# Optimization experiments

Hardware: AMD Instinct MI355X
Metric: run time of the kernel (lower is better)

Reference implementation:

```python
import jax, jax.numpy as jnp
import numpy as np
import math


def setup_inputs() -> dict:
    key = jax.random.key(0)
    kq, kk, kv = jax.random.split(key, 3)
    shape = (4, 16, 2048, 64)  # [B, H, S, D]
    return {
        "q": jax.random.normal(kq, shape, dtype=jnp.float32),
        "k": jax.random.normal(kk, shape, dtype=jnp.float32),
        "v": jax.random.normal(kv, shape, dtype=jnp.float32),
    }


def reference(q, k, v):
    # Faithful to the torch module: exp(QK^T / sqrt(d)) then row-normalize
    # (no max-subtraction, matching the original math exactly).
    d = q.shape[-1]
    a = jnp.einsum('bhid,bhjd->bhij', q, k)          # [B,H,S,S]
    a = jnp.exp(a / jnp.float32(math.sqrt(float(d))))
    d_inv = 1.0 / jnp.sum(a, axis=-1, keepdims=True)  # [B,H,S,1]
    a_hat = d_inv * a
    return jnp.einsum('bhij,bhjd->bhid', a_hat, v)   # [B,H,S,D]
```

## Files before the change

kernel.cpp:

```cpp
#include <hip/hip_runtime.h>
#include <hip/hip_fp16.h>

typedef _Float16 half8  __attribute__((ext_vector_type(8)));
typedef _Float16 half4  __attribute__((ext_vector_type(4)));
typedef __fp16   fp16x2 __attribute__((ext_vector_type(2)));
typedef float    floatx4 __attribute__((ext_vector_type(4)));
typedef float    f32x16 __attribute__((ext_vector_type(16)));
typedef unsigned int uint2v __attribute__((ext_vector_type(2)));
typedef unsigned int uint4v __attribute__((ext_vector_type(4)));

#define SEQ    2048
#define HD     64
#define QTILE  256
#define KVB    64
#define PITCH  72
#define NXCD   8

__global__ __launch_bounds__(256, 2)
void attn_fwd(const float* __restrict__ Q, const float* __restrict__ K,
              const float* __restrict__ V, float* __restrict__ O) {
    const int nqt  = SEQ / QTILE;

    const int bid  = blockIdx.x;
    const int xcd  = bid & (NXCD - 1);
    const int slot = bid >> 3;
    const int work = xcd * ((int)gridDim.x >> 3) + slot;
    const int head = work / nqt;
    const int qti  = work % nqt;

    const size_t hoff = (size_t)head * SEQ * HD;
    const float* Qh = Q + hoff;
    const float* Kh = K + hoff;
    const float* Vh = V + hoff;
    float*       Oh = O + hoff;

    const int tid  = threadIdx.x;
    const int lane = tid & 63;
    const int w    = tid >> 6;
    const int l31  = lane & 31;
    const int h    = lane >> 5;
    const int lg   = lane >> 4;
    const int lm   = lane & 15;

    __shared__ __align__(16) _Float16 lds[2][2][KVB][PITCH];

    const int q0w = qti * QTILE + w * 64;

    const int kr  = tid >> 4;
    const int kc  = (tid & 15) << 2;
    const int vr0 = w * 16 + lg * 4;

    const float QSCALE = 0.125f * 1.44269504f;
    half8 qf[2][4];
    #pragma unroll
    for (int set = 0; set < 2; ++set) {
        const float* qp = Qh + (size_t)(q0w + set*32 + l31) * HD + h*8;
        #pragma unroll
        for (int ks = 0; ks < 4; ++ks) {
            floatx4 a = *(const floatx4*)(qp + ks*16);
            floatx4 b = *(const floatx4*)(qp + ks*16 + 4);
            fp16x2 h0 = __builtin_amdgcn_cvt_pkrtz(a[0]*QSCALE, a[1]*QSCALE);
            fp16x2 h1 = __builtin_amdgcn_cvt_pkrtz(a[2]*QSCALE, a[3]*QSCALE);
            fp16x2 h2 = __builtin_amdgcn_cvt_pkrtz(b[0]*QSCALE, b[1]*QSCALE);
            fp16x2 h3 = __builtin_amdgcn_cvt_pkrtz(b[2]*QSCALE, b[3]*QSCALE);
            half8 hh;
            hh[0]=h0[0]; hh[1]=h0[1]; hh[2]=h1[0]; hh[3]=h1[1];
            hh[4]=h2[0]; hh[5]=h2[1]; hh[6]=h3[0]; hh[7]=h3[1];
            qf[set][ks] = hh;
        }
    }

    f32x16 Oa00 = {}, Oa01 = {}, Oa10 = {}, Oa11 = {};
    float ps0 = 0.f, ps1 = 0.f;

    floatx4 kp0, kp1, kp2, kp3;
    floatx4 vp0, vp1, vp2, vp3;

#define ISSUE(KV)                                                            \
    do {                                                                     \
        const float* kbp = Kh + (size_t)(KV) * HD;                           \
        kp0 = *(const floatx4*)(kbp + ( 0 + kr)*HD + kc);                    \
        kp1 = *(const floatx4*)(kbp + (16 + kr)*HD + kc);                    \
        kp2 = *(const floatx4*)(kbp + (32 + kr)*HD + kc);                    \
        kp3 = *(const floatx4*)(kbp + (48 + kr)*HD + kc);                    \
        const float* vbp = Vh + (size_t)(KV) * HD;                           \
        vp0[0] = vbp[(vr0+0)*HD +  0 + lm]; vp0[1] = vbp[(vr0+1)*HD +  0 + lm]; \
        vp0[2] = vbp[(vr0+2)*HD +  0 + lm]; vp0[3] = vbp[(vr0+3)*HD +  0 + lm]; \
        vp1[0] = vbp[(vr0+0)*HD + 16 + lm]; vp1[1] = vbp[(vr0+1)*HD + 16 + lm]; \
        vp1[2] = vbp[(vr0+2)*HD + 16 + lm]; vp1[3] = vbp[(vr0+3)*HD + 16 + lm]; \
        vp2[0] = vbp[(vr0+0)*HD + 32 + lm]; vp2[1] = vbp[(vr0+1)*HD + 32 + lm]; \
        vp2[2] = vbp[(vr0+2)*HD + 32 + lm]; vp2[3] = vbp[(vr0+3)*HD + 32 + lm]; \
        vp3[0] = vbp[(vr0+0)*HD + 48 + lm]; vp3[1] = vbp[(vr0+1)*HD + 48 + lm]; \
        vp3[2] = vbp[(vr0+2)*HD + 48 + lm]; vp3[3] = vbp[(vr0+3)*HD + 48 + lm]; \
    } while (0)

#define STORE_K(KB, REG, QUARTER)                                            \
    do {                                                                     \
        fp16x2 h0 = __builtin_amdgcn_cvt_pkrtz((REG)[0], (REG)[1]);          \
        fp16x2 h1 = __builtin_amdgcn_cvt_pkrtz((REG)[2], (REG)[3]);          \
        half4 kh; kh[0]=h0[0]; kh[1]=h0[1]; kh[2]=h1[0]; kh[3]=h1[1];        \
        *(half4*)&(KB)[((QUARTER)*16 + kr)*PITCH + kc] = kh;                 \
    } while (0)

#define STORE_V(VB, REG, QUARTER)                                            \
    do {                                                                     \
        fp16x2 h0 = __builtin_amdgcn_cvt_pkrtz((REG)[0], (REG)[1]);          \
        fp16x2 h1 = __builtin_amdgcn_cvt_pkrtz((REG)[2], (REG)[3]);          \
        half4 vh; vh[0]=h0[0]; vh[1]=h0[1]; vh[2]=h1[0]; vh[3]=h1[1];        \
        *(half4*)&(VB)[((QUARTER)*16 + lm)*PITCH + vr0] = vh;                \
    } while (0)

#define STORE_ALL(BUF)                                                       \
    do {                                                                     \
        _Float16* Kb_ = &lds[BUF][0][0][0];                                  \
        _Float16* Vb_ = &lds[BUF][1][0][0];                                  \
        STORE_K(Kb_, kp0, 0); STORE_K(Kb_, kp1, 1);                          \
        STORE_K(Kb_, kp2, 2); STORE_K(Kb_, kp3, 3);                          \
        STORE_V(Vb_, vp0, 0); STORE_V(Vb_, vp1, 1);                          \
        STORE_V(Vb_, vp2, 2); STORE_V(Vb_, vp3, 3);                          \
    } while (0)

#define EXP2(X) __builtin_amdgcn_exp2f(X)

#define EXPPACK(S, PW, PSUM)                                                 \
    do {                                                                     \
        float e0_=EXP2((S)[ 0]), e1_=EXP2((S)[ 1]), e2_=EXP2((S)[ 2]), e3_=EXP2((S)[ 3]); \
        float e4_=EXP2((S)[ 4]), e5_=EXP2((S)[ 5]), e6_=EXP2((S)[ 6]), e7_=EXP2((S)[ 7]); \
        float e8_=EXP2((S)[ 8]), e9_=EXP2((S)[ 9]), ea_=EXP2((S)[10]), eb_=EXP2((S)[11]); \
        float ec_=EXP2((S)[12]), ed_=EXP2((S)[13]), ee_=EXP2((S)[14]), ef_=EXP2((S)[15]); \
        PSUM += ((e0_+e1_)+(e2_+e3_)) + ((e4_+e5_)+(e6_+e7_))                \
              + ((e8_+e9_)+(ea_+eb_)) + ((ec_+ed_)+(ee_+ef_));               \
        unsigned x0_ = __builtin_bit_cast(unsigned, __builtin_amdgcn_cvt_pkrtz(e0_, e1_)); \
        unsigned x1_ = __builtin_bit_cast(unsigned, __builtin_amdgcn_cvt_pkrtz(e2_, e3_)); \
        unsigned y0_ = __builtin_bit_cast(unsigned, __builtin_amdgcn_cvt_pkrtz(e4_, e5_)); \
        unsigned y1_ = __builtin_bit_cast(unsigned, __builtin_amdgcn_cvt_pkrtz(e6_, e7_)); \
        unsigned z0_ = __builtin_bit_cast(unsigned, __builtin_amdgcn_cvt_pkrtz(e8_, e9_)); \
        unsigned z1_ = __builtin_bit_cast(unsigned, __builtin_amdgcn_cvt_pkrtz(ea_, eb_)); \
        unsigned u0_ = __builtin_bit_cast(unsigned, __builtin_amdgcn_cvt_pkrtz(ec_, ed_)); \
        unsigned u1_ = __builtin_bit_cast(unsigned, __builtin_amdgcn_cvt_pkrtz(ee_, ef_)); \
        uint2v r0_ = __builtin_amdgcn_permlane32_swap(x0_, y0_, false, false); \
        uint2v r1_ = __builtin_amdgcn_permlane32_swap(x1_, y1_, false, false); \
        uint2v r2_ = __builtin_amdgcn_permlane32_swap(z0_, u0_, false, false); \
        uint2v r3_ = __builtin_amdgcn_permlane32_swap(z1_, u1_, false, false); \
        PW[0] = r0_[0]; PW[1] = r1_[0]; PW[2] = r0_[1]; PW[3] = r1_[1];      \
        PW[4] = r2_[0]; PW[5] = r3_[0]; PW[6] = r2_[1]; PW[7] = r3_[1];      \
    } while (0)

    ISSUE(0);
    STORE_ALL(0);

    for (int kv = 0; kv < SEQ; kv += KVB) {
        const int buf = (kv >> 6) & 1;

        __syncthreads();

        {
            const int kvn = (kv + KVB < SEQ) ? (kv + KVB) : kv;
            ISSUE(kvn);
        }

        const _Float16* Kb = &lds[buf][0][0][0];
        const _Float16* Vb = &lds[buf][1][0][0];

        #pragma unroll
        for (int kb = 0; kb < 2; ++kb) {
            f32x16 s0 = {}, s1 = {};
            __builtin_amdgcn_s_setprio(1);
            #pragma unroll
            for (int ks = 0; ks < 4; ++ks) {
                half8 kf = *(const half8*)&Kb[(kb*32 + l31)*PITCH + ks*16 + h*8];
                s0 = __builtin_amdgcn_mfma_f32_32x32x16_f16(kf, qf[0][ks], s0, 0, 0, 0);
                s1 = __builtin_amdgcn_mfma_f32_32x32x16_f16(kf, qf[1][ks], s1, 0, 0, 0);
            }
            __builtin_amdgcn_s_setprio(0);

            unsigned pw0[8], pw1[8];
            EXPPACK(s0, pw0, ps0);
            EXPPACK(s1, pw1, ps1);

            __builtin_amdgcn_s_setprio(1);
            #pragma unroll
            for (int kh2 = 0; kh2 < 2; ++kh2) {
                const int ks = kb*2 + kh2;
                half8 vb0 = *(const half8*)&Vb[( 0 + l31)*PITCH + ks*16 + h*8];
                half8 vb1 = *(const half8*)&Vb[(32 + l31)*PITCH + ks*16 + h*8];
                uint4v a0 = { pw0[kh2*4+0], pw0[kh2*4+1], pw0[kh2*4+2], pw0[kh2*4+3] };
                uint4v a1 = { pw1[kh2*4+0], pw1[kh2*4+1], pw1[kh2*4+2], pw1[kh2*4+3] };
                half8 pa0 = __builtin_bit_cast(half8, a0);
                half8 pa1 = __builtin_bit_cast(half8, a1);
                Oa00 = __builtin_amdgcn_mfma_f32_32x32x16_f16(pa0, vb0, Oa00, 0, 0, 0);
                Oa01 = __builtin_amdgcn_mfma_f32_32x32x16_f16(pa0, vb1, Oa01, 0, 0, 0);
                Oa10 = __builtin_amdgcn_mfma_f32_32x32x16_f16(pa1, vb0, Oa10, 0, 0, 0);
                Oa11 = __builtin_amdgcn_mfma_f32_32x32x16_f16(pa1, vb1, Oa11, 0, 0, 0);
            }
            __builtin_amdgcn_s_setprio(0);
        }

        STORE_ALL(buf ^ 1);
    }
#undef ISSUE
#undef STORE_K
#undef STORE_V
#undef STORE_ALL
#undef EXPPACK
#undef EXP2

    ps0 += __shfl_xor(ps0, 32, 64);
    ps1 += __shfl_xor(ps1, 32, 64);

    #pragma unroll
    for (int r = 0; r < 16; ++r) {
        const int co = (r & 3) + 8*(r >> 2);
        float inv0 = 1.0f / __shfl(ps0, co + 4*h, 64);
        float inv1 = 1.0f / __shfl(ps1, co + 4*h, 64);
        const size_t row0 = (size_t)(q0w +      co + 4*h) * HD;
        const size_t row1 = (size_t)(q0w + 32 + co + 4*h) * HD;
        Oh[row0 +  0 + l31] = Oa00[r] * inv0;
        Oh[row0 + 32 + l31] = Oa01[r] * inv0;
        Oh[row1 +  0 + l31] = Oa10[r] * inv1;
        Oh[row1 + 32 + l31] = Oa11[r] * inv1;
    }
}

extern "C" void kernel_launch(void* const* d_in, const int* in_sizes, int n_in,
                              void* d_out, int out_size, void* d_ws, size_t ws_size,
                              hipStream_t stream) {
    const float* q = (const float*)d_in[0];
    const float* k = (const float*)d_in[1];
    const float* v = (const float*)d_in[2];
    float* o = (float*)d_out;
    int nheads  = in_sizes[0] / (SEQ * HD);
    int nblocks = nheads * (SEQ / QTILE);
    attn_fwd<<<nblocks, 256, 0, stream>>>(q, k, v, o);
}
```

Baseline: 88.47 us.

## Split global prefetch into phases interleaved with MFMA stages using workgroup barriers

Unrolls the per-tile loop into four explicit phases (QK half A, PV half A, QK half B, PV half B) and splits the next tile's global K/V prefetch into three pieces issued between them. Extra s_barrier calls after each phase keep the waves in lockstep, so memory loads from one wave overlap MFMA work from others in a ping-pong style. The main __syncthreads moves to after the LDS store. This adds several barriers per iteration and raises register pressure from preloading LDS fragments, which could stall waves or cut occupancy.

```diff
diff --git a/kernel.cpp b/kernel.cpp
--- a/kernel.cpp
+++ b/kernel.cpp
@@ -76,18 +76,27 @@
     floatx4 kp0, kp1, kp2, kp3;
     floatx4 vp0, vp1, vp2, vp3;
 
-#define ISSUE(KV)                                                            \
+#define ISSUE_K(KV)                                                          \
     do {                                                                     \
         const float* kbp = Kh + (size_t)(KV) * HD;                           \
         kp0 = *(const floatx4*)(kbp + ( 0 + kr)*HD + kc);                    \
         kp1 = *(const floatx4*)(kbp + (16 + kr)*HD + kc);                    \
         kp2 = *(const floatx4*)(kbp + (32 + kr)*HD + kc);                    \
         kp3 = *(const floatx4*)(kbp + (48 + kr)*HD + kc);                    \
+    } while (0)
+
+#define ISSUE_V1(KV)                                                         \
+    do {                                                                     \
         const float* vbp = Vh + (size_t)(KV) * HD;                           \
         vp0[0] = vbp[(vr0+0)*HD +  0 + lm]; vp0[1] = vbp[(vr0+1)*HD +  0 + lm]; \
         vp0[2] = vbp[(vr0+2)*HD +  0 + lm]; vp0[3] = vbp[(vr0+3)*HD +  0 + lm]; \
         vp1[0] = vbp[(vr0+0)*HD + 16 + lm]; vp1[1] = vbp[(vr0+1)*HD + 16 + lm]; \
         vp1[2] = vbp[(vr0+2)*HD + 16 + lm]; vp1[3] = vbp[(vr0+3)*HD + 16 + lm]; \
+    } while (0)
+
+#define ISSUE_V2(KV)                                                         \
+    do {                                                                     \
+        const float* vbp = Vh + (size_t)(KV) * HD;                           \
         vp2[0] = vbp[(vr0+0)*HD + 32 + lm]; vp2[1] = vbp[(vr0+1)*HD + 32 + lm]; \
         vp2[2] = vbp[(vr0+2)*HD + 32 + lm]; vp2[3] = vbp[(vr0+3)*HD + 32 + lm]; \
         vp3[0] = vbp[(vr0+0)*HD + 48 + lm]; vp3[1] = vbp[(vr0+1)*HD + 48 + lm]; \
@@ -146,59 +155,125 @@
         PW[4] = r2_[0]; PW[5] = r3_[0]; PW[6] = r2_[1]; PW[7] = r3_[1];      \
     } while (0)
 
-    ISSUE(0);
+    ISSUE_K(0); ISSUE_V1(0); ISSUE_V2(0);
     STORE_ALL(0);
+    __syncthreads();
 
     for (int kv = 0; kv < SEQ; kv += KVB) {
         const int buf = (kv >> 6) & 1;
-
-        __syncthreads();
-
-        {
-            const int kvn = (kv + KVB < SEQ) ? (kv + KVB) : kv;
-            ISSUE(kvn);
-        }
+        const int kvn = (kv + KVB < SEQ) ? (kv + KVB) : kv;
 
         const _Float16* Kb = &lds[buf][0][0][0];
         const _Float16* Vb = &lds[buf][1][0][0];
 
-        #pragma unroll
-        for (int kb = 0; kb < 2; ++kb) {
+        unsigned pw0[8], pw1[8], pw2[8], pw3[8];
+
+        {
+            half8 kA0 = *(const half8*)&Kb[( 0 + l31)*PITCH + 0*16 + h*8];
+            half8 kA1 = *(const half8*)&Kb[( 0 + l31)*PITCH + 1*16 + h*8];
+            half8 kA2 = *(const half8*)&Kb[( 0 + l31)*PITCH + 2*16 + h*8];
+            half8 kA3 = *(const half8*)&Kb[( 0 + l31)*PITCH + 3*16 + h*8];
+            ISSUE_K(kvn);
+            __builtin_amdgcn_s_barrier();
             f32x16 s0 = {}, s1 = {};
             __builtin_amdgcn_s_setprio(1);
-            #pragma unroll
-            for (int ks = 0; ks < 4; ++ks) {
-                half8 kf = *(const half8*)&Kb[(kb*32 + l31)*PITCH + ks*16 + h*8];
-                s0 = __builtin_amdgcn_mfma_f32_32x32x16_f16(kf, qf[0][ks], s0, 0, 0, 0);
-                s1 = __builtin_amdgcn_mfma_f32_32x32x16_f16(kf, qf[1][ks], s1, 0, 0, 0);
-            }
+            s0 = __builtin_amdgcn_mfma_f32_32x32x16_f16(kA0, qf[0][0], s0, 0, 0, 0);
+            s1 = __builtin_amdgcn_mfma_f32_32x32x16_f16(kA0, qf[1][0], s1, 0, 0, 0);
+            s0 = __builtin_amdgcn_mfma_f32_32x32x16_f16(kA1, qf[0][1], s0, 0, 0, 0);
+            s1 = __builtin_amdgcn_mfma_f32_32x32x16_f16(kA1, qf[1][1], s1, 0, 0, 0);
+            s0 = __builtin_amdgcn_mfma_f32_32x32x16_f16(kA2, qf[0][2], s0, 0, 0, 0);
+            s1 = __builtin_amdgcn_mfma_f32_32x32x16_f16(kA2, qf[1][2], s1, 0, 0, 0);
+            s0 = __builtin_amdgcn_mfma_f32_32x32x16_f16(kA3, qf[0][3], s0, 0, 0, 0);
+            s1 = __builtin_amdgcn_mfma_f32_32x32x16_f16(kA3, qf[1][3], s1, 0, 0, 0);
             __builtin_amdgcn_s_setprio(0);
-
-            unsigned pw0[8], pw1[8];
+            __builtin_amdgcn_s_barrier();
+
             EXPPACK(s0, pw0, ps0);
             EXPPACK(s1, pw1, ps1);
-
+        }
+        {
+            half8 vA0 = *(const half8*)&Vb[( 0 + l31)*PITCH + 0*16 + h*8];
+            half8 vA1 = *(const half8*)&Vb[(32 + l31)*PITCH + 0*16 + h*8];
+            half8 vA2 = *(const half8*)&Vb[( 0 + l31)*PITCH + 1*16 + h*8];
+            half8 vA3 = *(const half8*)&Vb[(32 + l31)*PITCH + 1*16 + h*8];
+            ISSUE_V1(kvn);
+            __builtin_amdgcn_s_barrier();
+            uint4v a0 = { pw0[0], pw0[1], pw0[2], pw0[3] };
+            uint4v a1 = { pw1[0], pw1[1], pw1[2], pw1[3] };
+            uint4v b0 = { pw0[4], pw0[5], pw0[6], pw0[7] };
+            uint4v b1 = { pw1[4], pw1[5], pw1[6], pw1[7] };
+            half8 pa0 = __builtin_bit_cast(half8, a0);
+            half8 pa1 = __builtin_bit_cast(half8, a1);
+            half8 pb0 = __builtin_bit_cast(half8, b0);
+            half8 pb1 = __builtin_bit_cast(half8, b1);
             __builtin_amdgcn_s_setprio(1);
-            #pragma unroll
-            for (int kh2 = 0; kh2 < 2; ++kh2) {
-                const int ks = kb*2 + kh2;
-                half8 vb0 = *(const half8*)&Vb[( 0 + l31)*PITCH + ks*16 + h*8];
-                half8 vb1 = *(const half8*)&Vb[(32 + l31)*PITCH + ks*16 + h*8];
-                uint4v a0 = { pw0[kh2*4+0], pw0[kh2*4+1], pw0[kh2*4+2], pw0[kh2*4+3] };
-                uint4v a1 = { pw1[kh2*4+0], pw1[kh2*4+1], pw1[kh2*4+2], pw1[kh2*4+3] };
-                half8 pa0 = __builtin_bit_cast(half8, a0);
-                half8 pa1 = __builtin_bit_cast(half8, a1);
-                Oa00 = __builtin_amdgcn_mfma_f32_32x32x16_f16(pa0, vb0, Oa00, 0, 0, 0);
-                Oa01 = __builtin_amdgcn_mfma_f32_32x32x16_f16(pa0, vb1, Oa01, 0, 0, 0);
-                Oa10 = __builtin_amdgcn_mfma_f32_32x32x16_f16(pa1, vb0, Oa10, 0, 0, 0);
-                Oa11 = __builtin_amdgcn_mfma_f32_32x32x16_f16(pa1, vb1, Oa11, 0, 0, 0);
-            }
+            Oa00 = __builtin_amdgcn_mfma_f32_32x32x16_f16(pa0, vA0, Oa00, 0, 0, 0);
+            Oa01 = __builtin_amdgcn_mfma_f32_32x32x16_f16(pa0, vA1, Oa01, 0, 0, 0);
+            Oa10 = __builtin_amdgcn_mfma_f32_32x32x16_f16(pa1, vA0, Oa10, 0, 0, 0);
+            Oa11 = __builtin_amdgcn_mfma_f32_32x32x16_f16(pa1, vA1, Oa11, 0, 0, 0);
+            Oa00 = __builtin_amdgcn_mfma_f32_32x32x16_f16(pb0, vA2, Oa00, 0, 0, 0);
+            Oa01 = __builtin_amdgcn_mfma_f32_32x32x16_f16(pb0, vA3, Oa01, 0, 0, 0);
+            Oa10 = __builtin_amdgcn_mfma_f32_32x32x16_f16(pb1, vA2, Oa10, 0, 0, 0);
+            Oa11 = __builtin_amdgcn_mfma_f32_32x32x16_f16(pb1, vA3, Oa11, 0, 0, 0);
             __builtin_amdgcn_s_setprio(0);
+            __builtin_amdgcn_s_barrier();
+        }
+
+        {
+            half8 kB0 = *(const half8*)&Kb[(32 + l31)*PITCH + 0*16 + h*8];
+            half8 kB1 = *(const half8*)&Kb[(32 + l31)*PITCH + 1*16 + h*8];
+            half8 kB2 = *(const half8*)&Kb[(32 + l31)*PITCH + 2*16 + h*8];
+            half8 kB3 = *(const half8*)&Kb[(32 + l31)*PITCH + 3*16 + h*8];
+            ISSUE_V2(kvn);
+            __builtin_amdgcn_s_barrier();
+            f32x16 s2 = {}, s3 = {};
+            __builtin_amdgcn_s_setprio(1);
+            s2 = __builtin_amdgcn_mfma_f32_32x32x16_f16(kB0, qf[0][0], s2, 0, 0, 0);
+            s3 = __builtin_amdgcn_mfma_f32_32x32x16_f16(kB0, qf[1][0], s3, 0, 0, 0);
+            s2 = __builtin_amdgcn_mfma_f32_32x32x16_f16(kB1, qf[0][1], s2, 0, 0, 0);
+            s3 = __builtin_amdgcn_mfma_f32_32x32x16_f16(kB1, qf[1][1], s3, 0, 0, 0);
+            s2 = __builtin_amdgcn_mfma_f32_32x32x16_f16(kB2, qf[0][2], s2, 0, 0, 0);
+            s3 = __builtin_amdgcn_mfma_f32_32x32x16_f16(kB2, qf[1][2], s3, 0, 0, 0);
+            s2 = __builtin_amdgcn_mfma_f32_32x32x16_f16(kB3, qf[0][3], s2, 0, 0, 0);
+            s3 = __builtin_amdgcn_mfma_f32_32x32x16_f16(kB3, qf[1][3], s3, 0, 0, 0);
+            __builtin_amdgcn_s_setprio(0);
+            __builtin_amdgcn_s_barrier();
+
+            EXPPACK(s2, pw2, ps0);
+            EXPPACK(s3, pw3, ps1);
+        }
+        {
+            half8 vB0 = *(const half8*)&Vb[( 0 + l31)*PITCH + 2*16 + h*8];
+            half8 vB1 = *(const half8*)&Vb[(32 + l31)*PITCH + 2*16 + h*8];
+            half8 vB2 = *(const half8*)&Vb[( 0 + l31)*PITCH + 3*16 + h*8];
+            half8 vB3 = *(const half8*)&Vb[(32 + l31)*PITCH + 3*16 + h*8];
+            __builtin_amdgcn_s_barrier();
+            uint4v a0 = { pw2[0], pw2[1], pw2[2], pw2[3] };
+            uint4v a1 = { pw3[0], pw3[1], pw3[2], pw3[3] };
+            uint4v b0 = { pw2[4], pw2[5], pw2[6], pw2[7] };
+            uint4v b1 = { pw3[4], pw3[5], pw3[6], pw3[7] };
+            half8 pa0 = __builtin_bit_cast(half8, a0);
+            half8 pa1 = __builtin_bit_cast(half8, a1);
+            half8 pb0 = __builtin_bit_cast(half8, b0);
+            half8 pb1 = __builtin_bit_cast(half8, b1);
+            __builtin_amdgcn_s_setprio(1);
+            Oa00 = __builtin_amdgcn_mfma_f32_32x32x16_f16(pa0, vB0, Oa00, 0, 0, 0);
+            Oa01 = __builtin_amdgcn_mfma_f32_32x32x16_f16(pa0, vB1, Oa01, 0, 0, 0);
+            Oa10 = __builtin_amdgcn_mfma_f32_32x32x16_f16(pa1, vB0, Oa10, 0, 0, 0);
+            Oa11 = __builtin_amdgcn_mfma_f32_32x32x16_f16(pa1, vB1, Oa11, 0, 0, 0);
+            Oa00 = __builtin_amdgcn_mfma_f32_32x32x16_f16(pb0, vB2, Oa00, 0, 0, 0);
+            Oa01 = __builtin_amdgcn_mfma_f32_32x32x16_f16(pb0, vB3, Oa01, 0, 0, 0);
+            Oa10 = __builtin_amdgcn_mfma_f32_32x32x16_f16(pb1, vB2, Oa10, 0, 0, 0);
+            Oa11 = __builtin_amdgcn_mfma_f32_32x32x16_f16(pb1, vB3, Oa11, 0, 0, 0);
+            __builtin_amdgcn_s_setprio(0);
         }
 
         STORE_ALL(buf ^ 1);
+        __syncthreads();
     }
-#undef ISSUE
+#undef ISSUE_K
+#undef ISSUE_V1
+#undef ISSUE_V2
 #undef STORE_K
 #undef STORE_V
 #undef STORE_ALL
```

After: 91.44 us. 1.03x slower.

## Double KV block to 128 and split global loads into two half-stages

Applied to the files above, without the earlier changes.

Raises the KV tile from 64 to 128 rows, so each iteration needs one barrier instead of two per 128 keys. Global loads for the next tile are issued in two halves, each overlapped with two 32-key compute sub-blocks and then stored to the other LDS buffer. V is stored transposed in a single wider-pitch array. LDS use roughly doubles, to about 72KB per block, which may limit the two-blocks-per-CU occupancy target, and the V pitch of 136 may cause bank conflicts.

```diff
diff --git a/kernel.cpp b/kernel.cpp
--- a/kernel.cpp
+++ b/kernel.cpp
@@ -12,8 +12,9 @@
 #define SEQ    2048
 #define HD     64
 #define QTILE  256
-#define KVB    64
-#define PITCH  72
+#define KVB    128
+#define KP     72
+#define VP     136
 #define NXCD   8
 
 __global__ __launch_bounds__(256, 2)
@@ -42,7 +43,8 @@
     const int lg   = lane >> 4;
     const int lm   = lane & 15;
 
-    __shared__ __align__(16) _Float16 lds[2][2][KVB][PITCH];
+    __shared__ __align__(16) _Float16 Klds[2][KVB][KP];
+    __shared__ __align__(16) _Float16 Vlds[2][HD][VP];
 
     const int q0w = qti * QTILE + w * 64;
 
@@ -76,14 +78,14 @@
     floatx4 kp0, kp1, kp2, kp3;
     floatx4 vp0, vp1, vp2, vp3;
 
-#define ISSUE(KV)                                                            \
-    do {                                                                     \
-        const float* kbp = Kh + (size_t)(KV) * HD;                           \
+#define ISSUE_H(KV, HALF)                                                    \
+    do {                                                                     \
+        const float* kbp = Kh + (size_t)((KV) + (HALF)*64) * HD;             \
         kp0 = *(const floatx4*)(kbp + ( 0 + kr)*HD + kc);                    \
         kp1 = *(const floatx4*)(kbp + (16 + kr)*HD + kc);                    \
         kp2 = *(const floatx4*)(kbp + (32 + kr)*HD + kc);                    \
         kp3 = *(const floatx4*)(kbp + (48 + kr)*HD + kc);                    \
-        const float* vbp = Vh + (size_t)(KV) * HD;                           \
+        const float* vbp = Vh + (size_t)((KV) + (HALF)*64) * HD;             \
         vp0[0] = vbp[(vr0+0)*HD +  0 + lm]; vp0[1] = vbp[(vr0+1)*HD +  0 + lm]; \
         vp0[2] = vbp[(vr0+2)*HD +  0 + lm]; vp0[3] = vbp[(vr0+3)*HD +  0 + lm]; \
         vp1[0] = vbp[(vr0+0)*HD + 16 + lm]; vp1[1] = vbp[(vr0+1)*HD + 16 + lm]; \
@@ -94,30 +96,42 @@
         vp3[2] = vbp[(vr0+2)*HD + 48 + lm]; vp3[3] = vbp[(vr0+3)*HD + 48 + lm]; \
     } while (0)
 
-#define STORE_K(KB, REG, QUARTER)                                            \
-    do {                                                                     \
-        fp16x2 h0 = __builtin_amdgcn_cvt_pkrtz((REG)[0], (REG)[1]);          \
-        fp16x2 h1 = __builtin_amdgcn_cvt_pkrtz((REG)[2], (REG)[3]);          \
-        half4 kh; kh[0]=h0[0]; kh[1]=h0[1]; kh[2]=h1[0]; kh[3]=h1[1];        \
-        *(half4*)&(KB)[((QUARTER)*16 + kr)*PITCH + kc] = kh;                 \
-    } while (0)
-
-#define STORE_V(VB, REG, QUARTER)                                            \
-    do {                                                                     \
-        fp16x2 h0 = __builtin_amdgcn_cvt_pkrtz((REG)[0], (REG)[1]);          \
-        fp16x2 h1 = __builtin_amdgcn_cvt_pkrtz((REG)[2], (REG)[3]);          \
-        half4 vh; vh[0]=h0[0]; vh[1]=h0[1]; vh[2]=h1[0]; vh[3]=h1[1];        \
-        *(half4*)&(VB)[((QUARTER)*16 + lm)*PITCH + vr0] = vh;                \
-    } while (0)
-
-#define STORE_ALL(BUF)                                                       \
-    do {                                                                     \
-        _Float16* Kb_ = &lds[BUF][0][0][0];                                  \
-        _Float16* Vb_ = &lds[BUF][1][0][0];                                  \
-        STORE_K(Kb_, kp0, 0); STORE_K(Kb_, kp1, 1);                          \
-        STORE_K(Kb_, kp2, 2); STORE_K(Kb_, kp3, 3);                          \
-        STORE_V(Vb_, vp0, 0); STORE_V(Vb_, vp1, 1);                          \
-        STORE_V(Vb_, vp2, 2); STORE_V(Vb_, vp3, 3);                          \
+#define STORE_H(BUF, HALF)                                                   \
+    do {                                                                     \
+        _Float16* Kb_ = &Klds[BUF][(HALF)*64][0];                            \
+        _Float16* Vb_ = &Vlds[BUF][0][0];                                    \
+        { fp16x2 h0 = __builtin_amdgcn_cvt_pkrtz(kp0[0], kp0[1]);            \
+          fp16x2 h1 = __builtin_amdgcn_cvt_pkrtz(kp0[2], kp0[3]);            \
+          half4 kh; kh[0]=h0[0]; kh[1]=h0[1]; kh[2]=h1[0]; kh[3]=h1[1];      \
+          *(half4*)&Kb_[( 0 + kr)*KP + kc] = kh; }                           \
+        { fp16x2 h0 = __builtin_amdgcn_cvt_pkrtz(kp1[0], kp1[1]);            \
+          fp16x2 h1 = __builtin_amdgcn_cvt_pkrtz(kp1[2], kp1[3]);            \
+          half4 kh; kh[0]=h0[0]; kh[1]=h0[1]; kh[2]=h1[0]; kh[3]=h1[1];      \
+          *(half4*)&Kb_[(16 + kr)*KP + kc] = kh; }                           \
+        { fp16x2 h0 = __builtin_amdgcn_cvt_pkrtz(kp2[0], kp2[1]);            \
+          fp16x2 h1 = __builtin_amdgcn_cvt_pkrtz(kp2[2], kp2[3]);            \
+          half4 kh; kh[0]=h0[0]; kh[1]=h0[1]; kh[2]=h1[0]; kh[3]=h1[1];      \
+          *(half4*)&Kb_[(32 + kr)*KP + kc] = kh; }                           \
+        { fp16x2 h0 = __builtin_amdgcn_cvt_pkrtz(kp3[0], kp3[1]);            \
+          fp16x2 h1 = __builtin_amdgcn_cvt_pkrtz(kp3[2], kp3[3]);            \
+          half4 kh; kh[0]=h0[0]; kh[1]=h0[1]; kh[2]=h1[0]; kh[3]=h1[1];      \
+          *(half4*)&Kb_[(48 + kr)*KP + kc] = kh; }                           \
+        { fp16x2 h0 = __builtin_amdgcn_cvt_pkrtz(vp0[0], vp0[1]);            \
+          fp16x2 h1 = __builtin_amdgcn_cvt_pkrtz(vp0[2], vp0[3]);            \
+          half4 vh; vh[0]=h0[0]; vh[1]=h0[1]; vh[2]=h1[0]; vh[3]=h1[1];      \
+          *(half4*)&Vb_[( 0 + lm)*VP + (HALF)*64 + vr0] = vh; }              \
+        { fp16x2 h0 = __builtin_amdgcn_cvt_pkrtz(vp1[0], vp1[1]);            \
+          fp16x2 h1 = __builtin_amdgcn_cvt_pkrtz(vp1[2], vp1[3]);            \
+          half4 vh; vh[0]=h0[0]; vh[1]=h0[1]; vh[2]=h1[0]; vh[3]=h1[1];      \
+          *(half4*)&Vb_[(16 + lm)*VP + (HALF)*64 + vr0] = vh; }              \
+        { fp16x2 h0 = __builtin_amdgcn_cvt_pkrtz(vp2[0], vp2[1]);            \
+          fp16x2 h1 = __builtin_amdgcn_cvt_pkrtz(vp2[2], vp2[3]);            \
+          half4 vh; vh[0]=h0[0]; vh[1]=h0[1]; vh[2]=h1[0]; vh[3]=h1[1];      \
+          *(half4*)&Vb_[(32 + lm)*VP + (HALF)*64 + vr0] = vh; }              \
+        { fp16x2 h0 = __builtin_amdgcn_cvt_pkrtz(vp3[0], vp3[1]);            \
+          fp16x2 h1 = __builtin_amdgcn_cvt_pkrtz(vp3[2], vp3[3]);            \
+          half4 vh; vh[0]=h0[0]; vh[1]=h0[1]; vh[2]=h1[0]; vh[3]=h1[1];      \
+          *(half4*)&Vb_[(48 + lm)*VP + (HALF)*64 + vr0] = vh; }              \
     } while (0)
 
 #define EXP2(X) __builtin_amdgcn_exp2f(X)
@@ -146,64 +160,66 @@
         PW[4] = r2_[0]; PW[5] = r3_[0]; PW[6] = r2_[1]; PW[7] = r3_[1];      \
     } while (0)
 
-    ISSUE(0);
-    STORE_ALL(0);
+#define COMPUTE_KB(KB)                                                       \
+    do {                                                                     \
+        f32x16 s0 = {}, s1 = {};                                             \
+        __builtin_amdgcn_s_setprio(1);                                       \
+        _Pragma("unroll")                                                    \
+        for (int ks = 0; ks < 4; ++ks) {                                     \
+            half8 kf = *(const half8*)&Kb[((KB)*32 + l31)*KP + ks*16 + h*8]; \
+            s0 = __builtin_amdgcn_mfma_f32_32x32x16_f16(kf, qf[0][ks], s0, 0, 0, 0); \
+            s1 = __builtin_amdgcn_mfma_f32_32x32x16_f16(kf, qf[1][ks], s1, 0, 0, 0); \
+        }                                                                    \
+        __builtin_amdgcn_s_setprio(0);                                       \
+        unsigned pw0[8], pw1[8];                                             \
+        EXPPACK(s0, pw0, ps0);                                               \
+        EXPPACK(s1, pw1, ps1);                                               \
+        __builtin_amdgcn_s_setprio(1);                                       \
+        _Pragma("unroll")                                                    \
+        for (int kh2 = 0; kh2 < 2; ++kh2) {                                  \
+            const int ks = (KB)*2 + kh2;                                     \
+            half8 vb0 = *(const half8*)&Vb[( 0 + l31)*VP + ks*16 + h*8];     \
+            half8 vb1 = *(const half8*)&Vb[(32 + l31)*VP + ks*16 + h*8];     \
+            uint4v a0 = { pw0[kh2*4+0], pw0[kh2*4+1], pw0[kh2*4+2], pw0[kh2*4+3] }; \
+            uint4v a1 = { pw1[kh2*4+0], pw1[kh2*4+1], pw1[kh2*4+2], pw1[kh2*4+3] }; \
+            half8 pa0 = __builtin_bit_cast(half8, a0);                       \
+            half8 pa1 = __builtin_bit_cast(half8, a1);                       \
+            Oa00 = __builtin_amdgcn_mfma_f32_32x32x16_f16(pa0, vb0, Oa00, 0, 0, 0); \
+            Oa01 = __builtin_amdgcn_mfma_f32_32x32x16_f16(pa0, vb1, Oa01, 0, 0, 0); \
+            Oa10 = __builtin_amdgcn_mfma_f32_32x32x16_f16(pa1, vb0, Oa10, 0, 0, 0); \
+            Oa11 = __builtin_amdgcn_mfma_f32_32x32x16_f16(pa1, vb1, Oa11, 0, 0, 0); \
+        }                                                                    \
+        __builtin_amdgcn_s_setprio(0);                                       \
+    } while (0)
+
+    ISSUE_H(0, 0); STORE_H(0, 0);
+    ISSUE_H(0, 1); STORE_H(0, 1);
+    __syncthreads();
 
     for (int kv = 0; kv < SEQ; kv += KVB) {
-        const int buf = (kv >> 6) & 1;
+        const int buf = (kv >> 7) & 1;
+        const int kvn = (kv + KVB < SEQ) ? (kv + KVB) : kv;
+
+        const _Float16* Kb = &Klds[buf][0][0];
+        const _Float16* Vb = &Vlds[buf][0][0];
+
+        ISSUE_H(kvn, 0);
+        COMPUTE_KB(0);
+        COMPUTE_KB(1);
+        STORE_H(buf ^ 1, 0);
+
+        ISSUE_H(kvn, 1);
+        COMPUTE_KB(2);
+        COMPUTE_KB(3);
+        STORE_H(buf ^ 1, 1);
 
         __syncthreads();
-
-        {
-            const int kvn = (kv + KVB < SEQ) ? (kv + KVB) : kv;
-            ISSUE(kvn);
-        }
-
-        const _Float16* Kb = &lds[buf][0][0][0];
-        const _Float16* Vb = &lds[buf][1][0][0];
-
-        #pragma unroll
-        for (int kb = 0; kb < 2; ++kb) {
-            f32x16 s0 = {}, s1 = {};
-            __builtin_amdgcn_s_setprio(1);
-            #pragma unroll
-            for (int ks = 0; ks < 4; ++ks) {
-                half8 kf = *(const half8*)&Kb[(kb*32 + l31)*PITCH + ks*16 + h*8];
-                s0 = __builtin_amdgcn_mfma_f32_32x32x16_f16(kf, qf[0][ks], s0, 0, 0, 0);
-                s1 = __builtin_amdgcn_mfma_f32_32x32x16_f16(kf, qf[1][ks], s1, 0, 0, 0);
-            }
-            __builtin_amdgcn_s_setprio(0);
-
-            unsigned pw0[8], pw1[8];
-            EXPPACK(s0, pw0, ps0);
-            EXPPACK(s1, pw1, ps1);
-
-            __builtin_amdgcn_s_setprio(1);
-            #pragma unroll
-            for (int kh2 = 0; kh2 < 2; ++kh2) {
-                const int ks = kb*2 + kh2;
-                half8 vb0 = *(const half8*)&Vb[( 0 + l31)*PITCH + ks*16 + h*8];
-                half8 vb1 = *(const half8*)&Vb[(32 + l31)*PITCH + ks*16 + h*8];
-                uint4v a0 = { pw0[kh2*4+0], pw0[kh2*4+1], pw0[kh2*4+2], pw0[kh2*4+3] };
-                uint4v a1 = { pw1[kh2*4+0], pw1[kh2*4+1], pw1[kh2*4+2], pw1[kh2*4+3] };
-                half8 pa0 = __builtin_bit_cast(half8, a0);
-                half8 pa1 = __builtin_bit_cast(half8, a1);
-                Oa00 = __builtin_amdgcn_mfma_f32_32x32x16_f16(pa0, vb0, Oa00, 0, 0, 0);
-                Oa01 = __builtin_amdgcn_mfma_f32_32x32x16_f16(pa0, vb1, Oa01, 0, 0, 0);
-                Oa10 = __builtin_amdgcn_mfma_f32_32x32x16_f16(pa1, vb0, Oa10, 0, 0, 0);
-                Oa11 = __builtin_amdgcn_mfma_f32_32x32x16_f16(pa1, vb1, Oa11, 0, 0, 0);
-            }
-            __builtin_amdgcn_s_setprio(0);
-        }
-
-        STORE_ALL(buf ^ 1);
     }
-#undef ISSUE
-#undef STORE_K
-#undef STORE_V
-#undef STORE_ALL
+#undef ISSUE_H
+#undef STORE_H
 #undef EXPPACK
 #undef EXP2
+#undef COMPUTE_KB
 
     ps0 += __shfl_xor(ps0, 32, 64);
     ps1 += __shfl_xor(ps1, 32, 64);
```

New measurement: 349.6 us. +295.1%, slower.
